# Kernel optimization log

Hardware: AMD Instinct MI355X
Metric: run time of the kernel (lower is better)

Reference implementation:

```python
import jax, jax.numpy as jnp
import numpy as np

B, T, N, D, NH = 4, 256, 8, 128, 4
SCALES = (1, 2, 3, 5)
LAGS = (1, 2, 3)
MLP_H = 32
NL_SCALE = 0.1
CMIN, CMAX = -2.5, 2.0
L_ENC = 2  # num_attn_layers


def _ln(x, g, b, eps=1e-5):
    m = x.mean(-1, keepdims=True)
    v = ((x - m) ** 2).mean(-1, keepdims=True)
    return (x - m) * jax.lax.rsqrt(v + eps) * g + b


def _gelu(x):
    return jax.nn.gelu(x, approximate=False)


def _mha(q, k, v, Wq, bq, Wk, bk, Wv, bv, Wo, bo, nh):
    Bq, Lq, Dm = q.shape
    Lk = k.shape[1]
    hd = Dm // nh
    qh = (q @ Wq.T + bq).reshape(Bq, Lq, nh, hd).transpose(0, 2, 1, 3)
    kh = (k @ Wk.T + bk).reshape(Bq, Lk, nh, hd).transpose(0, 2, 1, 3)
    vh = (v @ Wv.T + bv).reshape(Bq, Lk, nh, hd).transpose(0, 2, 1, 3)
    s = jnp.einsum('bhqd,bhkd->bhqk', qh, kh) / jnp.sqrt(jnp.float32(hd))
    p = jax.nn.softmax(s, axis=-1)
    o = jnp.einsum('bhqk,bhkd->bhqd', p, vh).transpose(0, 2, 1, 3).reshape(Bq, Lq, Dm)
    return o @ Wo.T + bo


def setup_inputs() -> dict:
    key = jax.random.key(0)
    ks = jax.random.split(key, 24)
    def w(k, shape, s=0.02):
        return s * jax.random.normal(k, shape, jnp.float32)
    inp = {}
    inp['visible_states'] = jax.random.uniform(ks[0], (B, T, N), jnp.float32) + 0.05
    inp['state_emb'] = jax.random.normal(ks[1], (B, T, N, D), jnp.float32)
    # LearnedBaseline params
    inp['r5'] = 0.1 * jnp.ones((N,), jnp.float32)
    A = 0.02 * jax.random.normal(ks[2], (N, N), jnp.float32)
    inp['A55'] = A.at[jnp.arange(N), jnp.arange(N)].set(-0.2)
    inp['bl_bias'] = jnp.zeros((N,), jnp.float32)
    inp['nl_W1'] = w(ks[3], (MLP_H, N), 0.1); inp['nl_b1'] = jnp.zeros((MLP_H,), jnp.float32)
    inp['nl_W2'] = w(ks[4], (N, MLP_H), 0.1); inp['nl_b2'] = jnp.zeros((N,), jnp.float32)
    # ResidualEncoder input MLP
    IN_DIM = len(SCALES) * (1 + len(LAGS))  # 16
    inp['mlp_W1'] = w(ks[5], (D, IN_DIM), 0.1); inp['mlp_b1'] = jnp.zeros((D,), jnp.float32)
    inp['mlp_W2'] = w(ks[6], (D, D)); inp['mlp_b2'] = jnp.zeros((D,), jnp.float32)
    inp['mlp_ln_g'] = jnp.ones((D,), jnp.float32); inp['mlp_ln_b'] = jnp.zeros((D,), jnp.float32)
    # ResidualEncoder transformer layers (stacked over L_ENC layers)
    inp['enc_qkv_W'] = w(ks[7], (L_ENC, 3 * D, D)); inp['enc_qkv_b'] = jnp.zeros((L_ENC, 3 * D), jnp.float32)
    inp['enc_out_W'] = w(ks[8], (L_ENC, D, D)); inp['enc_out_b'] = jnp.zeros((L_ENC, D), jnp.float32)
    inp['enc_ln1_g'] = jnp.ones((L_ENC, D), jnp.float32); inp['enc_ln1_b'] = jnp.zeros((L_ENC, D), jnp.float32)
    inp['enc_ff_W1'] = w(ks[9], (L_ENC, 2 * D, D)); inp['enc_ff_b1'] = jnp.zeros((L_ENC, 2 * D), jnp.float32)
    inp['enc_ff_W2'] = w(ks[10], (L_ENC, D, 2 * D)); inp['enc_ff_b2'] = jnp.zeros((L_ENC, D), jnp.float32)
    inp['enc_ln2_g'] = jnp.ones((L_ENC, D), jnp.float32); inp['enc_ln2_b'] = jnp.zeros((L_ENC, D), jnp.float32)
    # CrossAttentionFusion
    inp['ca_Wq'] = w(ks[11], (D, D)); inp['ca_bq'] = jnp.zeros((D,), jnp.float32)
    inp['ca_Wk'] = w(ks[12], (D, D)); inp['ca_bk'] = jnp.zeros((D,), jnp.float32)
    inp['ca_Wv'] = w(ks[13], (D, D)); inp['ca_bv'] = jnp.zeros((D,), jnp.float32)
    inp['ca_Wo'] = w(ks[14], (D, D)); inp['ca_bo'] = jnp.zeros((D,), jnp.float32)
    inp['ca_ln1_g'] = jnp.ones((D,), jnp.float32); inp['ca_ln1_b'] = jnp.zeros((D,), jnp.float32)
    inp['ca_ff_W1'] = w(ks[15], (4 * D, 2 * D)); inp['ca_ff_b1'] = jnp.zeros((4 * D,), jnp.float32)
    inp['ca_ff_W2'] = w(ks[16], (D, 4 * D)); inp['ca_ff_b2'] = jnp.zeros((D,), jnp.float32)
    inp['ca_ln2_g'] = jnp.ones((D,), jnp.float32); inp['ca_ln2_b'] = jnp.zeros((D,), jnp.float32)
    return inp


def _forward(visible_states, state_emb, r5, A55, bl_bias, nl_W1, nl_b1, nl_W2, nl_b2,
             mlp_W1, mlp_b1, mlp_W2, mlp_b2, mlp_ln_g, mlp_ln_b,
             enc_qkv_W, enc_qkv_b, enc_out_W, enc_out_b, enc_ln1_g, enc_ln1_b,
             enc_ff_W1, enc_ff_b1, enc_ff_W2, enc_ff_b2, enc_ln2_g, enc_ln2_b,
             ca_Wq, ca_bq, ca_Wk, ca_bk, ca_Wv, ca_bv, ca_Wo, ca_bo,
             ca_ln1_g, ca_ln1_b, ca_ff_W1, ca_ff_b1, ca_ff_W2, ca_ff_b2,
             ca_ln2_g, ca_ln2_b):
    # ---- LearnedBaseline on x_t = visible_states[:, :-1] ----
    safe = jnp.clip(visible_states, 1e-6, None)
    logx = jnp.log(safe)
    x_t = visible_states[:, :-1]  # (B,T-1,N)
    lin = r5 + jnp.einsum('btn,mn->btm', x_t, A55)
    nl = _gelu(x_t @ nl_W1.T + nl_b1) @ nl_W2.T + nl_b2
    b1 = lin + NL_SCALE * nl + bl_bias  # (B,T-1,N)
    # ---- MultiScaleResidual ----
    res_list = []
    for k in SCALES:
        actual = jnp.clip(logx[:, k:] - logx[:, :-k], CMIN * k, CMAX * k)  # (B,T-k,N)
        bk = b1[:, 0:T - k]
        for i in range(1, k):
            bk = bk + b1[:, i:i + T - k]
        res = actual - bk
        res_list.append(jnp.pad(res, ((0, 0), (0, k), (0, 0))))
    residuals = jnp.stack(res_list, axis=-1)  # (B,T,N,S)
    # ---- ResidualEncoder: takens delays ----
    feats = [residuals] + [jnp.pad(residuals, ((0, 0), (lag, 0), (0, 0), (0, 0)))[:, :T]
                           for lag in LAGS]
    x = jnp.concatenate(feats, axis=-1)  # (B,T,N,16)
    x = _gelu(x @ mlp_W1.T + mlp_b1)
    x = _gelu(x @ mlp_W2.T + mlp_b2)
    x = _ln(x, mlp_ln_g, mlp_ln_b)
    # sinusoidal PE over time
    pos = jnp.arange(T, dtype=jnp.float32)[:, None]
    div = jnp.exp(jnp.arange(0, D, 2, dtype=jnp.float32) * (-jnp.log(10000.0) / D))
    pe = jnp.stack([jnp.sin(pos * div), jnp.cos(pos * div)], axis=-1).reshape(T, D)
    x = x + pe[None, :, None, :]
    # temporal self-attention over (B*N, T, D)
    xt = x.transpose(0, 2, 1, 3).reshape(B * N, T, D)
    for i in range(L_ENC):
        Wq, Wk, Wv = jnp.split(enc_qkv_W[i], 3, axis=0)
        bq, bk_, bv = jnp.split(enc_qkv_b[i], 3)
        a = _mha(xt, xt, xt, Wq, bq, Wk, bk_, Wv, bv, enc_out_W[i], enc_out_b[i], NH)
        xt = _ln(xt + a, enc_ln1_g[i], enc_ln1_b[i])
        ff = _gelu(xt @ enc_ff_W1[i].T + enc_ff_b1[i]) @ enc_ff_W2[i].T + enc_ff_b2[i]
        xt = _ln(xt + ff, enc_ln2_g[i], enc_ln2_b[i])
    residual_emb = xt.reshape(B, N, T, D).transpose(0, 2, 1, 3)  # (B,T,N,D)
    # ---- CrossAttentionFusion ----
    s = state_emb.reshape(B, T * N, D)
    r = residual_emb.reshape(B, T * N, D)
    a = _mha(s, r, r, ca_Wq, ca_bq, ca_Wk, ca_bk, ca_Wv, ca_bv, ca_Wo, ca_bo, NH)
    s = _ln(s + a, ca_ln1_g, ca_ln1_b)
    fused = _gelu(jnp.concatenate([s, r], axis=-1) @ ca_ff_W1.T + ca_ff_b1) @ ca_ff_W2.T + ca_ff_b2
    out = _ln(s + fused, ca_ln2_g, ca_ln2_b)
    return out.reshape(B, T, N, D)


def reference(visible_states, state_emb, r5, A55, bl_bias, nl_W1, nl_b1, nl_W2, nl_b2,
              mlp_W1, mlp_b1, mlp_W2, mlp_b2, mlp_ln_g, mlp_ln_b,
              enc_qkv_W, enc_qkv_b, enc_out_W, enc_out_b, enc_ln1_g, enc_ln1_b,
              enc_ff_W1, enc_ff_b1, enc_ff_W2, enc_ff_b2, enc_ln2_g, enc_ln2_b,
              ca_Wq, ca_bq, ca_Wk, ca_bk, ca_Wv, ca_bv, ca_Wo, ca_bo,
              ca_ln1_g, ca_ln1_b, ca_ff_W1, ca_ff_b1, ca_ff_W2, ca_ff_b2,
              ca_ln2_g, ca_ln2_b):
    return _forward(visible_states, state_emb, r5, A55, bl_bias, nl_W1, nl_b1, nl_W2, nl_b2,
                    mlp_W1, mlp_b1, mlp_W2, mlp_b2, mlp_ln_g, mlp_ln_b,
                    enc_qkv_W, enc_qkv_b, enc_out_W, enc_out_b, enc_ln1_g, enc_ln1_b,
                    enc_ff_W1, enc_ff_b1, enc_ff_W2, enc_ff_b2, enc_ln2_g, enc_ln2_b,
                    ca_Wq, ca_bq, ca_Wk, ca_bk, ca_Wv, ca_bv, ca_Wo, ca_bo,
                    ca_ln1_g, ca_ln1_b, ca_ff_W1, ca_ff_b1, ca_ff_W2, ca_ff_b2,
                    ca_ln2_g, ca_ln2_b)
```

## Files before the change

kernel.cpp:

```cpp
#include <hip/hip_runtime.h>
#include <math.h>

#define B_ 4
#define T_ 256
#define N_ 8
#define D_ 128
#define NH_ 4
#define HD_ 32
#define LENC_ 2
#define MLPH_ 32
#define NL_SCALE_ 0.1f

typedef __bf16 bf16;
typedef __attribute__((ext_vector_type(2))) __bf16 bf16x2;
typedef __attribute__((ext_vector_type(4))) __bf16 bf16x4;
typedef __attribute__((ext_vector_type(8))) __bf16 bf16x8;
typedef __attribute__((ext_vector_type(4))) float f32x4;

__device__ __forceinline__ f32x4 pv_mfma16(bf16x4 a, bf16x4 b, f32x4 c) {
#if __has_builtin(__builtin_amdgcn_mfma_f32_16x16x16_bf16)
    return __builtin_amdgcn_mfma_f32_16x16x16_bf16(a, b, c, 0, 0, 0);
#else
    typedef __attribute__((ext_vector_type(4))) short s4;
    union U { bf16x4 h; s4 s; };
    U ua, ub; ua.h = a; ub.h = b;
    return __builtin_amdgcn_mfma_f32_16x16x16bf16_1k(ua.s, ub.s, c, 0, 0, 0);
#endif
}

__device__ __forceinline__ float gelu_f(float x) {
    return 0.5f * x * (1.0f + erff(x * 0.7071067811865476f));
}

__global__ void k_prep(const float* __restrict__ eqkvW, const float* __restrict__ eoutW,
                       const float* __restrict__ eff1, const float* __restrict__ eff2,
                       const float* __restrict__ wq, const float* __restrict__ wk,
                       const float* __restrict__ wv, const float* __restrict__ wo,
                       const float* __restrict__ cff1, const float* __restrict__ cff2,
                       const float* __restrict__ mlpW2, const float* __restrict__ semb,
                       const float* __restrict__ bk, const float* __restrict__ bv,
                       bf16* __restrict__ Wpk, bf16* __restrict__ sembh,
                       float* __restrict__ bpk) {
    int i = blockIdx.x * 256 + threadIdx.x;
    if (i < 540672) {
        const float* src; int off;
        if      (i < 98304)  { src = eqkvW; off = 0; }
        else if (i < 131072) { src = eoutW; off = 98304; }
        else if (i < 196608) { src = eff1;  off = 131072; }
        else if (i < 262144) { src = eff2;  off = 196608; }
        else if (i < 278528) { src = wq;    off = 262144; }
        else if (i < 294912) { src = wk;    off = 278528; }
        else if (i < 311296) { src = wv;    off = 294912; }
        else if (i < 327680) { src = wo;    off = 311296; }
        else if (i < 458752) { src = cff1;  off = 327680; }
        else if (i < 524288) { src = cff2;  off = 458752; }
        else                 { src = mlpW2; off = 524288; }
        Wpk[i] = (bf16)src[i - off];
    } else if (i < 540672 + 1048576) {
        int j = i - 540672;
        sembh[j] = (bf16)semb[j];
    } else if (i < 540672 + 1048576 + 256) {
        int t = i - 540672 - 1048576;
        bpk[t] = (t < 128) ? bk[t] : bv[t - 128];
    }
}

__global__ void k_b1(const float* __restrict__ vs, const float* __restrict__ r5,
                     const float* __restrict__ A55, const float* __restrict__ bl_bias,
                     const float* __restrict__ nlW1, const float* __restrict__ nlb1,
                     const float* __restrict__ nlW2, const float* __restrict__ nlb2,
                     float* __restrict__ b1w) {
    int idx = blockIdx.x * blockDim.x + threadIdx.x;
    if (idx >= B_ * (T_ - 1)) return;
    int b = idx / (T_ - 1), t = idx % (T_ - 1);
    float x[N_];
    for (int n = 0; n < N_; n++) x[n] = vs[(b * T_ + t) * N_ + n];
    float h[MLPH_];
    for (int j = 0; j < MLPH_; j++) {
        float a = nlb1[j];
        for (int n = 0; n < N_; n++) a += x[n] * nlW1[j * N_ + n];
        h[j] = gelu_f(a);
    }
    for (int m = 0; m < N_; m++) {
        float lin = r5[m];
        for (int n = 0; n < N_; n++) lin += x[n] * A55[m * N_ + n];
        float nl = nlb2[m];
        for (int j = 0; j < MLPH_; j++) nl += h[j] * nlW2[m * MLPH_ + j];
        b1w[idx * N_ + m] = lin + NL_SCALE_ * nl + bl_bias[m];
    }
}

__global__ void k_mlp1(const float* __restrict__ vs, const float* __restrict__ b1w,
                       const float* __restrict__ W1, const float* __restrict__ b1,
                       bf16* __restrict__ H1h) {
    int tok = blockIdx.x;
    int d = threadIdx.x;
    int b = tok >> 11, t = (tok >> 3) & 255, n = tok & 7;
    __shared__ float f[16];
    if (d < 16) {
        const int SC[4] = {1, 2, 3, 5};
        int lag = d >> 2, si = d & 3, k = SC[si];
        int tp = t - lag;
        float r = 0.0f;
        if (tp >= 0 && tp < T_ - k) {
            float lx0 = logf(fmaxf(vs[(b * T_ + tp) * N_ + n], 1e-6f));
            float lx1 = logf(fmaxf(vs[(b * T_ + tp + k) * N_ + n], 1e-6f));
            float a = lx1 - lx0;
            a = fminf(fmaxf(a, -2.5f * (float)k), 2.0f * (float)k);
            float bk = 0.0f;
            for (int i = 0; i < k; i++) bk += b1w[(b * (T_ - 1) + tp + i) * N_ + n];
            r = a - bk;
        }
        f[d] = r;
    }
    __syncthreads();
    float a = b1[d];
    const float* w = W1 + d * 16;
#pragma unroll
    for (int c = 0; c < 16; c++) a += f[c] * w[c];
    H1h[(size_t)tok * 128 + d] = (bf16)gelu_f(a);
}

__global__ __launch_bounds__(256) void k_gemm4(
    const bf16* __restrict__ A, const bf16* __restrict__ W,
    const float* __restrict__ bias, float* __restrict__ Cf,
    bf16* __restrict__ Ch, bf16* __restrict__ dq, bf16* __restrict__ dk,
    bf16* __restrict__ dvv, int M, int N, int K, int act, int mode) {
    int lane = threadIdx.x & 63;
    int wv = threadIdx.x >> 6;
    int c = lane & 15, g = lane >> 4;
    int nN = N >> 6;
    int tn = blockIdx.x % nN, tm = blockIdx.x / nN;
    int row0 = tm * 64 + wv * 16;
    int cb = tn * 64;

    const bf16x8* Ap  = (const bf16x8*)(A + (size_t)(row0 + c) * K) + g;
    const bf16x8* Wp0 = (const bf16x8*)(W + (size_t)(cb + c) * K) + g;
    const bf16x8* Wp1 = (const bf16x8*)(W + (size_t)(cb + 16 + c) * K) + g;
    const bf16x8* Wp2 = (const bf16x8*)(W + (size_t)(cb + 32 + c) * K) + g;
    const bf16x8* Wp3 = (const bf16x8*)(W + (size_t)(cb + 48 + c) * K) + g;
    f32x4 a0 = {0, 0, 0, 0}, a1 = {0, 0, 0, 0};
    f32x4 a2 = {0, 0, 0, 0}, a3 = {0, 0, 0, 0};
    int nk = K >> 5;
    for (int k = 0; k < nk; k++) {
        bf16x8 av = Ap[k * 4];
        a0 = __builtin_amdgcn_mfma_f32_16x16x32_bf16(av, Wp0[k * 4], a0, 0, 0, 0);
        a1 = __builtin_amdgcn_mfma_f32_16x16x32_bf16(av, Wp1[k * 4], a1, 0, 0, 0);
        a2 = __builtin_amdgcn_mfma_f32_16x16x32_bf16(av, Wp2[k * 4], a2, 0, 0, 0);
        a3 = __builtin_amdgcn_mfma_f32_16x16x32_bf16(av, Wp3[k * 4], a3, 0, 0, 0);
    }
    int rowb = row0 + g * 4;
#pragma unroll
    for (int ct = 0; ct < 4; ct++) {
        f32x4 acc = (ct == 0) ? a0 : (ct == 1) ? a1 : (ct == 2) ? a2 : a3;
        int col = cb + ct * 16 + c;
        float bvv = bias[col];
#pragma unroll
        for (int i = 0; i < 4; i++) {
            float v = acc[i] + bvv;
            if (act) v = gelu_f(v);
            int row = rowb + i;
            if (mode == 0) {
                if (Cf) Cf[(size_t)row * N + col] = v;
                if (Ch) Ch[(size_t)row * N + col] = (bf16)v;
            } else if (mode == 1) {
                int s = row >> 8, t = row & 255;
                int h = (col >> 5) & 3, d = col & 31;
                int sh = s * 4 + h;
                if (col < 128)      dq[((size_t)sh * 256 + t) * 32 + d] = (bf16)v;
                else if (col < 256) dk[((size_t)sh * 256 + t) * 32 + d] = (bf16)v;
                else                dvv[((size_t)sh * 32 + d) * 256 + t] = (bf16)v;
            } else if (mode == 2) {
                int b = row >> 11, ll = row & 2047;
                int h = col >> 5, d = col & 31;
                dq[((size_t)(b * 4 + h) * 2048 + ll) * 32 + d] = (bf16)v;
            } else {
                int b = row >> 11, n = (row >> 8) & 7, t = row & 255;
                int ll = t * 8 + n;
                int h = (col >> 5) & 3, d = col & 31;
                if (col < 128) dk[((size_t)(b * 4 + h) * 2048 + ll) * 32 + d] = (bf16)v;
                else           dvv[((size_t)(b * 4 + h) * 32 + d) * 2048 + ll] = (bf16)v;
            }
        }
    }
}

__global__ __launch_bounds__(256) void k_gemm_ln(
    const bf16* __restrict__ A, const bf16* __restrict__ W,
    const float* __restrict__ bias, int K,
    const float* __restrict__ resf,
    const float* __restrict__ g, const float* __restrict__ be,
    float* __restrict__ outf, bf16* __restrict__ outh, int hs,
    const bf16* __restrict__ catsrc, int flags) {
    __shared__ float S[32][132];
    int tid = threadIdx.x;
    int w = tid >> 6, lane = tid & 63;
    int c = lane & 15, gq = lane >> 4;
    int r0 = blockIdx.x * 32 + (w >> 1) * 16;
    int cb = (w & 1) * 64;

    const bf16x8* Ap  = (const bf16x8*)(A + (size_t)(r0 + c) * K) + gq;
    const bf16x8* Wp0 = (const bf16x8*)(W + (size_t)(cb + c) * K) + gq;
    const bf16x8* Wp1 = (const bf16x8*)(W + (size_t)(cb + 16 + c) * K) + gq;
    const bf16x8* Wp2 = (const bf16x8*)(W + (size_t)(cb + 32 + c) * K) + gq;
    const bf16x8* Wp3 = (const bf16x8*)(W + (size_t)(cb + 48 + c) * K) + gq;
    f32x4 a0 = {0, 0, 0, 0}, a1 = {0, 0, 0, 0};
    f32x4 a2 = {0, 0, 0, 0}, a3 = {0, 0, 0, 0};
    int nk = K >> 5;
    for (int k = 0; k < nk; k++) {
        bf16x8 av = Ap[k * 4];
        a0 = __builtin_amdgcn_mfma_f32_16x16x32_bf16(av, Wp0[k * 4], a0, 0, 0, 0);
        a1 = __builtin_amdgcn_mfma_f32_16x16x32_bf16(av, Wp1[k * 4], a1, 0, 0, 0);
        a2 = __builtin_amdgcn_mfma_f32_16x16x32_bf16(av, Wp2[k * 4], a2, 0, 0, 0);
        a3 = __builtin_amdgcn_mfma_f32_16x16x32_bf16(av, Wp3[k * 4], a3, 0, 0, 0);
    }
    int lrow = (w >> 1) * 16 + gq * 4;
    float b0 = bias[cb + c], b1v = bias[cb + 16 + c];
    float b2v = bias[cb + 32 + c], b3v = bias[cb + 48 + c];
#pragma unroll
    for (int r = 0; r < 4; r++) {
        float v0 = a0[r] + b0, v1 = a1[r] + b1v;
        float v2 = a2[r] + b2v, v3 = a3[r] + b3v;
        if (flags & 1) {
            v0 = gelu_f(v0); v1 = gelu_f(v1); v2 = gelu_f(v2); v3 = gelu_f(v3);
        }
        S[lrow + r][cb + c] = v0;       S[lrow + r][cb + 16 + c] = v1;
        S[lrow + r][cb + 32 + c] = v2;  S[lrow + r][cb + 48 + c] = v3;
    }
    __syncthreads();

    int row = tid >> 3, cg = tid & 7;
    int grow = blockIdx.x * 32 + row;
    int b = grow >> 11, t = (grow >> 3) & 255, n = grow & 7;
    int orow = (flags & 4) ? ((b * 8 + n) * 256 + t) : grow;
    float v[16];
#pragma unroll
    for (int j = 0; j < 16; j++) v[j] = S[row][cg * 16 + j];
    if (resf) {
        const float4* rp = (const float4*)(resf + (size_t)grow * 128 + cg * 16);
#pragma unroll
        for (int j4 = 0; j4 < 4; j4++) {
            float4 rv = rp[j4];
            v[4 * j4 + 0] += rv.x; v[4 * j4 + 1] += rv.y;
            v[4 * j4 + 2] += rv.z; v[4 * j4 + 3] += rv.w;
        }
    }
    float s = 0.0f;
#pragma unroll
    for (int j = 0; j < 16; j++) s += v[j];
    s += __shfl_xor(s, 1); s += __shfl_xor(s, 2); s += __shfl_xor(s, 4);
    float mean = s * (1.0f / 128.0f);
    float vs = 0.0f;
#pragma unroll
    for (int j = 0; j < 16; j++) { float d = v[j] - mean; vs += d * d; }
    vs += __shfl_xor(vs, 1); vs += __shfl_xor(vs, 2); vs += __shfl_xor(vs, 4);
    float rstd = rsqrtf(vs * (1.0f / 128.0f) + 1e-5f);
    float y[16];
#pragma unroll
    for (int j = 0; j < 16; j++) {
        int col = cg * 16 + j;
        y[j] = (v[j] - mean) * rstd * g[col] + be[col];
    }
    if (flags & 2) {
#pragma unroll
        for (int jj = 0; jj < 8; jj++) {
            int j2 = cg * 8 + jj;
            float freq = expf((float)(2 * j2) * (-9.210340371976184f / 128.0f));
            float ang = (float)t * freq;
            y[2 * jj] += sinf(ang);
            y[2 * jj + 1] += cosf(ang);
        }
    }
    if (outf) {
        float4* op = (float4*)(outf + (size_t)orow * 128 + cg * 16);
#pragma unroll
        for (int j4 = 0; j4 < 4; j4++) {
            float4 o; o.x = y[4 * j4]; o.y = y[4 * j4 + 1];
            o.z = y[4 * j4 + 2]; o.w = y[4 * j4 + 3];
            op[j4] = o;
        }
    }
    if (outh) {
        bf16x8* op = (bf16x8*)(outh + (size_t)orow * hs + cg * 16);
#pragma unroll
        for (int j8 = 0; j8 < 2; j8++) {
            bf16x8 o;
#pragma unroll
            for (int e = 0; e < 8; e++) o[e] = (bf16)y[8 * j8 + e];
            op[j8] = o;
        }
        if (catsrc) {
            const bf16x8* cp = (const bf16x8*)(
                catsrc + ((size_t)(b * 8 + n) * 256 + t) * 128 + cg * 16);
            bf16x8* dp = (bf16x8*)(outh + (size_t)orow * 256 + 128 + cg * 16);
            dp[0] = cp[0]; dp[1] = cp[1];
        }
    }
}

__global__ __launch_bounds__(256) void k_mattn(
    const bf16* __restrict__ Qh, const bf16* __restrict__ Kh,
    const bf16* __restrict__ Vth, bf16* __restrict__ ATTh,
    int Lq, int Lk, int NSH) {
    int sh = blockIdx.x % NSH;
    int qblk = blockIdx.x / NSH;
    int wv = threadIdx.x >> 6;
    int lane = threadIdx.x & 63;
    int c = lane & 15, g = lane >> 4;
    int q0 = qblk * 64;

    __shared__ float O_lds[4][64][36];
    __shared__ float L_lds[4][64];

    const float scale = 0.17677669529663687f;
    const f32x4 zero = {0, 0, 0, 0};

    bf16x8 bq[4];
#pragma unroll
    for (int qt = 0; qt < 4; qt++)
        bq[qt] = *(const bf16x8*)(
            Qh + ((size_t)sh * Lq + q0 + qt * 16 + c) * 32 + g * 8);

    int klen = Lk >> 2;
    int kbeg = wv * klen;
    const bf16* Kbase = Kh + (size_t)sh * Lk * 32 + (size_t)kbeg * 32;
    const bf16* Vbase = Vth + (size_t)sh * 32 * Lk + kbeg;

    f32x4 oT[4][2];
#pragma unroll
    for (int qt = 0; qt < 4; qt++) { oT[qt][0] = zero; oT[qt][1] = zero; }
    float lsum[4] = {0, 0, 0, 0};

    int ntiles = klen >> 5;
    bf16x8 ka = *(const bf16x8*)(Kbase + (size_t)c * 32 + g * 8);
    bf16x8 kb = *(const bf16x8*)(Kbase + (size_t)(16 + c) * 32 + g * 8);
    bf16x4 va0 = *(const bf16x4*)(Vbase + (size_t)c * Lk + g * 4);
    bf16x4 va1 = *(const bf16x4*)(Vbase + (size_t)c * Lk + 16 + g * 4);
    bf16x4 vb0 = *(const bf16x4*)(Vbase + (size_t)(16 + c) * Lk + g * 4);
    bf16x4 vb1 = *(const bf16x4*)(Vbase + (size_t)(16 + c) * Lk + 16 + g * 4);

    for (int t = 0; t < ntiles; t++) {
        bf16x8 cka = ka, ckb = kb;
        bf16x4 cva0 = va0, cva1 = va1, cvb0 = vb0, cvb1 = vb1;
        int nk0 = ((t + 1 < ntiles) ? (t + 1) : t) << 5;
        ka = *(const bf16x8*)(Kbase + (size_t)(nk0 + c) * 32 + g * 8);
        kb = *(const bf16x8*)(Kbase + (size_t)(nk0 + 16 + c) * 32 + g * 8);
        va0 = *(const bf16x4*)(Vbase + (size_t)c * Lk + nk0 + g * 4);
        va1 = *(const bf16x4*)(Vbase + (size_t)c * Lk + nk0 + 16 + g * 4);
        vb0 = *(const bf16x4*)(Vbase + (size_t)(16 + c) * Lk + nk0 + g * 4);
        vb1 = *(const bf16x4*)(Vbase + (size_t)(16 + c) * Lk + nk0 + 16 + g * 4);

#pragma unroll
        for (int qt = 0; qt < 4; qt++) {
            f32x4 s0 = __builtin_amdgcn_mfma_f32_16x16x32_bf16(cka, bq[qt], zero, 0, 0, 0);
            f32x4 s1 = __builtin_amdgcn_mfma_f32_16x16x32_bf16(ckb, bq[qt], zero, 0, 0, 0);
            bf16x4 p0, p1;
#pragma unroll
            for (int r = 0; r < 4; r++) {
                float e0 = __expf(s0[r] * scale);
                float e1 = __expf(s1[r] * scale);
                lsum[qt] += e0 + e1;
                p0[r] = (bf16)e0;
                p1[r] = (bf16)e1;
            }
            oT[qt][0] = pv_mfma16(cva0, p0, oT[qt][0]);
            oT[qt][0] = pv_mfma16(cva1, p1, oT[qt][0]);
            oT[qt][1] = pv_mfma16(cvb0, p0, oT[qt][1]);
            oT[qt][1] = pv_mfma16(cvb1, p1, oT[qt][1]);
        }
    }

#pragma unroll
    for (int qt = 0; qt < 4; qt++) {
        float s = lsum[qt];
        s += __shfl_xor(s, 16);
        s += __shfl_xor(s, 32);
        if (g == 0) L_lds[wv][qt * 16 + c] = s;
        *(f32x4*)&O_lds[wv][qt * 16 + c][g * 4] = oT[qt][0];
        *(f32x4*)&O_lds[wv][qt * 16 + c][16 + g * 4] = oT[qt][1];
    }
    __syncthreads();

    int tid = threadIdx.x;
    int ql = tid >> 2, dq = (tid & 3) * 8;
    float ltot = L_lds[0][ql] + L_lds[1][ql] + L_lds[2][ql] + L_lds[3][ql];
    float inv = 1.0f / ltot;
    float acc[8];
#pragma unroll
    for (int j = 0; j < 8; j++) acc[j] = 0.0f;
#pragma unroll
    for (int w = 0; w < 4; w++) {
        const float* p = &O_lds[w][ql][dq];
#pragma unroll
        for (int j = 0; j < 8; j++) acc[j] += p[j];
    }
    int h = sh & 3, sb = sh >> 2;
    bf16x8 o;
#pragma unroll
    for (int j = 0; j < 8; j++) o[j] = (bf16)(acc[j] * inv);
    *(bf16x8*)(ATTh + ((size_t)sb * Lq + q0 + ql) * 128 + h * 32 + dq) = o;
}

extern "C" void kernel_launch(void* const* d_in, const int* in_sizes, int n_in,
                              void* d_out, int out_size, void* d_ws, size_t ws_size,
                              hipStream_t stream) {
    const float* vs       = (const float*)d_in[0];
    const float* semb     = (const float*)d_in[1];
    const float* r5       = (const float*)d_in[2];
    const float* A55      = (const float*)d_in[3];
    const float* bl_bias  = (const float*)d_in[4];
    const float* nl_W1    = (const float*)d_in[5];
    const float* nl_b1    = (const float*)d_in[6];
    const float* nl_W2    = (const float*)d_in[7];
    const float* nl_b2    = (const float*)d_in[8];
    const float* mlp_W1   = (const float*)d_in[9];
    const float* mlp_b1   = (const float*)d_in[10];
    const float* mlp_W2   = (const float*)d_in[11];
    const float* mlp_b2   = (const float*)d_in[12];
    const float* mlp_ln_g = (const float*)d_in[13];
    const float* mlp_ln_b = (const float*)d_in[14];
    const float* enc_qkv_W = (const float*)d_in[15];
    const float* enc_qkv_b = (const float*)d_in[16];
    const float* enc_out_W = (const float*)d_in[17];
    const float* enc_out_b = (const float*)d_in[18];
    const float* enc_ln1_g = (const float*)d_in[19];
    const float* enc_ln1_b = (const float*)d_in[20];
    const float* enc_ff_W1 = (const float*)d_in[21];
    const float* enc_ff_b1 = (const float*)d_in[22];
    const float* enc_ff_W2 = (const float*)d_in[23];
    const float* enc_ff_b2 = (const float*)d_in[24];
    const float* enc_ln2_g = (const float*)d_in[25];
    const float* enc_ln2_b = (const float*)d_in[26];
    const float* ca_Wq = (const float*)d_in[27];
    const float* ca_bq = (const float*)d_in[28];
    const float* ca_Wk = (const float*)d_in[29];
    const float* ca_bk = (const float*)d_in[30];
    const float* ca_Wv = (const float*)d_in[31];
    const float* ca_bv = (const float*)d_in[32];
    const float* ca_Wo = (const float*)d_in[33];
    const float* ca_bo = (const float*)d_in[34];
    const float* ca_ln1_g = (const float*)d_in[35];
    const float* ca_ln1_b = (const float*)d_in[36];
    const float* ca_ff_W1 = (const float*)d_in[37];
    const float* ca_ff_b1 = (const float*)d_in[38];
    const float* ca_ff_W2 = (const float*)d_in[39];
    const float* ca_ff_b2 = (const float*)d_in[40];
    const float* ca_ln2_g = (const float*)d_in[41];
    const float* ca_ln2_b = (const float*)d_in[42];
    float* out = (float*)d_out;

    char* base = (char*)d_ws;
    float* b1w   = (float*)(base + 0);
    float* X0    = (float*)(base + 163840);
    float* X1    = (float*)(base + 4358144);
    char*  QKVr  = base + 8552448;
    bf16*  Wpk   = (bf16*) (base + 25329664);
    float* bpk   = (float*)(base + 26411008);
    bf16*  X0h   = (bf16*) (base + 26412032);
    bf16*  X1h   = (bf16*) (base + 28509184);
    bf16*  sembh = (bf16*) (base + 30606336);
    bf16*  ATTh  = (bf16*) (base + 32703488);
    bf16*  Qh    = (bf16*)QKVr;
    bf16*  Kh    = (bf16*)(QKVr + 2097152);
    bf16*  Vth   = (bf16*)(QKVr + 4194304);
    bf16*  CATh  = (bf16*)QKVr;
    bf16*  Hh    = (bf16*)(QKVr + 4194304);

    const int NTOK = B_ * T_ * N_;

    k_prep<<<dim3(6209), dim3(256), 0, stream>>>(
        enc_qkv_W, enc_out_W, enc_ff_W1, enc_ff_W2, ca_Wq, ca_Wk, ca_Wv, ca_Wo,
        ca_ff_W1, ca_ff_W2, mlp_W2, semb, ca_bk, ca_bv, Wpk, sembh, bpk);

    k_b1<<<dim3((B_ * (T_ - 1) + 63) / 64), dim3(64), 0, stream>>>(
        vs, r5, A55, bl_bias, nl_W1, nl_b1, nl_W2, nl_b2, b1w);
    k_mlp1<<<dim3(NTOK), dim3(128), 0, stream>>>(vs, b1w, mlp_W1, mlp_b1,
                                                 (bf16*)X1h);
    k_gemm_ln<<<dim3(256), dim3(256), 0, stream>>>(
        (bf16*)X1h, Wpk + 524288, mlp_b2, 128, nullptr, mlp_ln_g, mlp_ln_b,
        X0, X0h, 128, nullptr, 1 | 2 | 4);

    for (int i = 0; i < LENC_; i++) {
        k_gemm4<<<dim3(768), dim3(256), 0, stream>>>(
            X0h, Wpk + i * 49152, enc_qkv_b + i * 384, nullptr, nullptr,
            Qh, Kh, Vth, NTOK, 384, 128, 0, 1);
        k_mattn<<<dim3(512), dim3(256), 0, stream>>>(
            Qh, Kh, Vth, ATTh, 256, 256, 128);
        k_gemm_ln<<<dim3(256), dim3(256), 0, stream>>>(
            ATTh, Wpk + 98304 + i * 16384, enc_out_b + i * 128, 128, X0,
            enc_ln1_g + i * 128, enc_ln1_b + i * 128, X1, X1h, 128, nullptr, 0);
        k_gemm4<<<dim3(512), dim3(256), 0, stream>>>(
            X1h, Wpk + 131072 + i * 32768, enc_ff_b1 + i * 256, nullptr, Hh,
            nullptr, nullptr, nullptr, NTOK, 256, 128, 1, 0);
        k_gemm_ln<<<dim3(256), dim3(256), 0, stream>>>(
            Hh, Wpk + 196608 + i * 32768, enc_ff_b2 + i * 128, 256, X1,
            enc_ln2_g + i * 128, enc_ln2_b + i * 128, X0, X0h, 128, nullptr, 0);
    }

    k_gemm4<<<dim3(256), dim3(256), 0, stream>>>(
        sembh, Wpk + 262144, ca_bq, nullptr, nullptr, Qh, nullptr, nullptr,
        NTOK, 128, 128, 0, 2);
    k_gemm4<<<dim3(512), dim3(256), 0, stream>>>(
        X0h, Wpk + 278528, bpk, nullptr, nullptr, nullptr, Kh, Vth,
        NTOK, 256, 128, 0, 3);
    k_mattn<<<dim3(512), dim3(256), 0, stream>>>(
        Qh, Kh, Vth, ATTh, 2048, 2048, 16);
    k_gemm_ln<<<dim3(256), dim3(256), 0, stream>>>(
        ATTh, Wpk + 311296, ca_bo, 128, semb, ca_ln1_g, ca_ln1_b,
        X1, CATh, 256, X0h, 0);
    k_gemm4<<<dim3(1024), dim3(256), 0, stream>>>(
        CATh, Wpk + 327680, ca_ff_b1, nullptr, Hh, nullptr, nullptr, nullptr,
        NTOK, 512, 256, 1, 0);
    k_gemm_ln<<<dim3(256), dim3(256), 0, stream>>>(
        Hh, Wpk + 458752, ca_ff_b2, 512, X1, ca_ln2_g, ca_ln2_b,
        out, nullptr, 128, nullptr, 0);
}
```

Before: 373.9 us.

## Fuse attention output, LayerNorm and FFN into single per-tile tail kernels

Each encoder layer's out-projection, residual LayerNorm, FFN up-projection with GELU, down-projection and second LayerNorm now run in one kernel per 32-row tile, with intermediates held in shared memory rather than written to global buffers. The cross-attention tail gets the same treatment, building the concatenated FFN input in registers from the LN output and the encoder output. The cross-attention Q and KV projections are merged into one launch as well. This removes several kernel launches and global round trips of the hidden activations. In exchange, each tile's FFN weights are reread by every block, shared-memory use per block is higher, and only 256 blocks do the larger FFN GEMMs, so parallelism drops. The cross tail's second residual now uses the bf16 copy of the LN output rather than the fp32 one.

```diff
diff --git a/kernel.cpp b/kernel.cpp
--- a/kernel.cpp
+++ b/kernel.cpp
@@ -121,16 +121,16 @@
     H1h[(size_t)tok * 128 + d] = (bf16)gelu_f(a);
 }
 
-__global__ __launch_bounds__(256) void k_gemm4(
-    const bf16* __restrict__ A, const bf16* __restrict__ W,
+__device__ __forceinline__ void gemm4_body(
+    int bid, const bf16* __restrict__ A, const bf16* __restrict__ W,
     const float* __restrict__ bias, float* __restrict__ Cf,
     bf16* __restrict__ Ch, bf16* __restrict__ dq, bf16* __restrict__ dk,
-    bf16* __restrict__ dvv, int M, int N, int K, int act, int mode) {
+    bf16* __restrict__ dvv, int N, int K, int act, int mode) {
     int lane = threadIdx.x & 63;
     int wv = threadIdx.x >> 6;
     int c = lane & 15, g = lane >> 4;
     int nN = N >> 6;
-    int tn = blockIdx.x % nN, tm = blockIdx.x / nN;
+    int tn = bid % nN, tm = bid / nN;
     int row0 = tm * 64 + wv * 16;
     int cb = tn * 64;
 
@@ -185,13 +185,33 @@
     }
 }
 
+__global__ __launch_bounds__(256) void k_gemm4(
+    const bf16* __restrict__ A, const bf16* __restrict__ W,
+    const float* __restrict__ bias, bf16* __restrict__ dq,
+    bf16* __restrict__ dk, bf16* __restrict__ dvv, int N, int K, int mode) {
+    gemm4_body(blockIdx.x, A, W, bias, nullptr, nullptr, dq, dk, dvv,
+               N, K, 0, mode);
+}
+
+__global__ __launch_bounds__(256) void k_qkvc(
+    const bf16* __restrict__ sembh, const bf16* __restrict__ Wq,
+    const float* __restrict__ bq, const bf16* __restrict__ X0h,
+    const bf16* __restrict__ Wkv, const float* __restrict__ bkv,
+    bf16* __restrict__ Qh, bf16* __restrict__ Kh, bf16* __restrict__ Vth) {
+    if (blockIdx.x < 256)
+        gemm4_body(blockIdx.x, sembh, Wq, bq, nullptr, nullptr,
+                   Qh, nullptr, nullptr, 128, 128, 0, 2);
+    else
+        gemm4_body(blockIdx.x - 256, X0h, Wkv, bkv, nullptr, nullptr,
+                   nullptr, Kh, Vth, 256, 128, 0, 3);
+}
+
 __global__ __launch_bounds__(256) void k_gemm_ln(
     const bf16* __restrict__ A, const bf16* __restrict__ W,
     const float* __restrict__ bias, int K,
     const float* __restrict__ resf,
     const float* __restrict__ g, const float* __restrict__ be,
-    float* __restrict__ outf, bf16* __restrict__ outh, int hs,
-    const bf16* __restrict__ catsrc, int flags) {
+    float* __restrict__ outf, bf16* __restrict__ outh, int hs, int flags) {
     __shared__ float S[32][132];
     int tid = threadIdx.x;
     int w = tid >> 6, lane = tid & 63;
@@ -289,11 +309,357 @@
             for (int e = 0; e < 8; e++) o[e] = (bf16)y[8 * j8 + e];
             op[j8] = o;
         }
-        if (catsrc) {
-            const bf16x8* cp = (const bf16x8*)(
-                catsrc + ((size_t)(b * 8 + n) * 256 + t) * 128 + cg * 16);
-            bf16x8* dp = (bf16x8*)(outh + (size_t)orow * 256 + 128 + cg * 16);
-            dp[0] = cp[0]; dp[1] = cp[1];
+    }
+}
+
+__global__ __launch_bounds__(256) void k_enc_tail(
+    const bf16* __restrict__ ATTh, const bf16* __restrict__ Wo,
+    const float* __restrict__ bo, const float* __restrict__ X0res,
+    const float* __restrict__ g1, const float* __restrict__ be1,
+    const bf16* __restrict__ W1, const float* __restrict__ bf1,
+    const bf16* __restrict__ W2, const float* __restrict__ bf2,
+    const float* __restrict__ g2, const float* __restrict__ be2,
+    float* __restrict__ X0out, bf16* __restrict__ X0hout) {
+    __shared__ float S[32][132];
+    __shared__ float X1f[32][132];
+    __shared__ bf16 X1h[32][136];
+    __shared__ bf16 H[32][264];
+    int tid = threadIdx.x;
+    int w = tid >> 6, lane = tid & 63;
+    int c = lane & 15, gq = lane >> 4;
+    int r0l = (w >> 1) * 16;
+    int cb = (w & 1) * 64;
+    int blk = blockIdx.x;
+    const f32x4 zero = {0, 0, 0, 0};
+
+    {
+        const bf16x8* Ap  = (const bf16x8*)(ATTh + (size_t)(blk * 32 + r0l + c) * 128) + gq;
+        const bf16x8* Wp0 = (const bf16x8*)(Wo + (size_t)(cb + c) * 128) + gq;
+        const bf16x8* Wp1 = (const bf16x8*)(Wo + (size_t)(cb + 16 + c) * 128) + gq;
+        const bf16x8* Wp2 = (const bf16x8*)(Wo + (size_t)(cb + 32 + c) * 128) + gq;
+        const bf16x8* Wp3 = (const bf16x8*)(Wo + (size_t)(cb + 48 + c) * 128) + gq;
+        f32x4 a0 = zero, a1 = zero, a2 = zero, a3 = zero;
+#pragma unroll
+        for (int k = 0; k < 4; k++) {
+            bf16x8 av = Ap[k * 4];
+            a0 = __builtin_amdgcn_mfma_f32_16x16x32_bf16(av, Wp0[k * 4], a0, 0, 0, 0);
+            a1 = __builtin_amdgcn_mfma_f32_16x16x32_bf16(av, Wp1[k * 4], a1, 0, 0, 0);
+            a2 = __builtin_amdgcn_mfma_f32_16x16x32_bf16(av, Wp2[k * 4], a2, 0, 0, 0);
+            a3 = __builtin_amdgcn_mfma_f32_16x16x32_bf16(av, Wp3[k * 4], a3, 0, 0, 0);
+        }
+        int lrow = r0l + gq * 4;
+        float b0 = bo[cb + c], b1v = bo[cb + 16 + c];
+        float b2v = bo[cb + 32 + c], b3v = bo[cb + 48 + c];
+#pragma unroll
+        for (int r = 0; r < 4; r++) {
+            S[lrow + r][cb + c] = a0[r] + b0;
+            S[lrow + r][cb + 16 + c] = a1[r] + b1v;
+            S[lrow + r][cb + 32 + c] = a2[r] + b2v;
+            S[lrow + r][cb + 48 + c] = a3[r] + b3v;
+        }
+    }
+    __syncthreads();
+    {
+        int row = tid >> 3, cg = tid & 7;
+        float v[16];
+        const float4* rp = (const float4*)(X0res + (size_t)(blk * 32 + row) * 128 + cg * 16);
+#pragma unroll
+        for (int j4 = 0; j4 < 4; j4++) {
+            float4 rv = rp[j4];
+            v[4 * j4 + 0] = S[row][cg * 16 + 4 * j4 + 0] + rv.x;
+            v[4 * j4 + 1] = S[row][cg * 16 + 4 * j4 + 1] + rv.y;
+            v[4 * j4 + 2] = S[row][cg * 16 + 4 * j4 + 2] + rv.z;
+            v[4 * j4 + 3] = S[row][cg * 16 + 4 * j4 + 3] + rv.w;
+        }
+        float s = 0.0f;
+#pragma unroll
+        for (int j = 0; j < 16; j++) s += v[j];
+        s += __shfl_xor(s, 1); s += __shfl_xor(s, 2); s += __shfl_xor(s, 4);
+        float mean = s * (1.0f / 128.0f);
+        float vs = 0.0f;
+#pragma unroll
+        for (int j = 0; j < 16; j++) { float d = v[j] - mean; vs += d * d; }
+        vs += __shfl_xor(vs, 1); vs += __shfl_xor(vs, 2); vs += __shfl_xor(vs, 4);
+        float rstd = rsqrtf(vs * (1.0f / 128.0f) + 1e-5f);
+#pragma unroll
+        for (int j = 0; j < 16; j++) {
+            int col = cg * 16 + j;
+            float y = (v[j] - mean) * rstd * g1[col] + be1[col];
+            X1f[row][col] = y;
+            X1h[row][col] = (bf16)y;
+        }
+    }
+    __syncthreads();
+    {
+        bf16x8 af[4];
+#pragma unroll
+        for (int k = 0; k < 4; k++)
+            af[k] = *(const bf16x8*)&X1h[r0l + c][k * 32 + gq * 8];
+#pragma unroll
+        for (int ci = 0; ci < 2; ci++) {
+            int cb2 = cb + ci * 128;
+            const bf16x8* Wp0 = (const bf16x8*)(W1 + (size_t)(cb2 + c) * 128) + gq;
+            const bf16x8* Wp1 = (const bf16x8*)(W1 + (size_t)(cb2 + 16 + c) * 128) + gq;
+            const bf16x8* Wp2 = (const bf16x8*)(W1 + (size_t)(cb2 + 32 + c) * 128) + gq;
+            const bf16x8* Wp3 = (const bf16x8*)(W1 + (size_t)(cb2 + 48 + c) * 128) + gq;
+            f32x4 a0 = zero, a1 = zero, a2 = zero, a3 = zero;
+#pragma unroll
+            for (int k = 0; k < 4; k++) {
+                a0 = __builtin_amdgcn_mfma_f32_16x16x32_bf16(af[k], Wp0[k * 4], a0, 0, 0, 0);
+                a1 = __builtin_amdgcn_mfma_f32_16x16x32_bf16(af[k], Wp1[k * 4], a1, 0, 0, 0);
+                a2 = __builtin_amdgcn_mfma_f32_16x16x32_bf16(af[k], Wp2[k * 4], a2, 0, 0, 0);
+                a3 = __builtin_amdgcn_mfma_f32_16x16x32_bf16(af[k], Wp3[k * 4], a3, 0, 0, 0);
+            }
+            int lrow = r0l + gq * 4;
+#pragma unroll
+            for (int r = 0; r < 4; r++) {
+                H[lrow + r][cb2 + c]      = (bf16)gelu_f(a0[r] + bf1[cb2 + c]);
+                H[lrow + r][cb2 + 16 + c] = (bf16)gelu_f(a1[r] + bf1[cb2 + 16 + c]);
+                H[lrow + r][cb2 + 32 + c] = (bf16)gelu_f(a2[r] + bf1[cb2 + 32 + c]);
+                H[lrow + r][cb2 + 48 + c] = (bf16)gelu_f(a3[r] + bf1[cb2 + 48 + c]);
+            }
+        }
+    }
+    __syncthreads();
+    {
+        bf16x8 af[8];
+#pragma unroll
+        for (int k = 0; k < 8; k++)
+            af[k] = *(const bf16x8*)&H[r0l + c][k * 32 + gq * 8];
+        const bf16x8* Wp0 = (const bf16x8*)(W2 + (size_t)(cb + c) * 256) + gq;
+        const bf16x8* Wp1 = (const bf16x8*)(W2 + (size_t)(cb + 16 + c) * 256) + gq;
+        const bf16x8* Wp2 = (const bf16x8*)(W2 + (size_t)(cb + 32 + c) * 256) + gq;
+        const bf16x8* Wp3 = (const bf16x8*)(W2 + (size_t)(cb + 48 + c) * 256) + gq;
+        f32x4 a0 = zero, a1 = zero, a2 = zero, a3 = zero;
+#pragma unroll
+        for (int k = 0; k < 8; k++) {
+            a0 = __builtin_amdgcn_mfma_f32_16x16x32_bf16(af[k], Wp0[k * 4], a0, 0, 0, 0);
+            a1 = __builtin_amdgcn_mfma_f32_16x16x32_bf16(af[k], Wp1[k * 4], a1, 0, 0, 0);
+            a2 = __builtin_amdgcn_mfma_f32_16x16x32_bf16(af[k], Wp2[k * 4], a2, 0, 0, 0);
+            a3 = __builtin_amdgcn_mfma_f32_16x16x32_bf16(af[k], Wp3[k * 4], a3, 0, 0, 0);
+        }
+        int lrow = r0l + gq * 4;
+        float b0 = bf2[cb + c], b1v = bf2[cb + 16 + c];
+        float b2v = bf2[cb + 32 + c], b3v = bf2[cb + 48 + c];
+#pragma unroll
+        for (int r = 0; r < 4; r++) {
+            S[lrow + r][cb + c] = a0[r] + b0;
+            S[lrow + r][cb + 16 + c] = a1[r] + b1v;
+            S[lrow + r][cb + 32 + c] = a2[r] + b2v;
+            S[lrow + r][cb + 48 + c] = a3[r] + b3v;
+        }
+    }
+    __syncthreads();
+    {
+        int row = tid >> 3, cg = tid & 7;
+        float v[16];
+#pragma unroll
+        for (int j = 0; j < 16; j++)
+            v[j] = S[row][cg * 16 + j] + X1f[row][cg * 16 + j];
+        float s = 0.0f;
+#pragma unroll
+        for (int j = 0; j < 16; j++) s += v[j];
+        s += __shfl_xor(s, 1); s += __shfl_xor(s, 2); s += __shfl_xor(s, 4);
+        float mean = s * (1.0f / 128.0f);
+        float vs = 0.0f;
+#pragma unroll
+        for (int j = 0; j < 16; j++) { float d = v[j] - mean; vs += d * d; }
+        vs += __shfl_xor(vs, 1); vs += __shfl_xor(vs, 2); vs += __shfl_xor(vs, 4);
+        float rstd = rsqrtf(vs * (1.0f / 128.0f) + 1e-5f);
+        size_t grow = (size_t)(blk * 32 + row);
+        float4* of = (float4*)(X0out + grow * 128 + cg * 16);
+        bf16x8* oh = (bf16x8*)(X0hout + grow * 128 + cg * 16);
+        float y[16];
+#pragma unroll
+        for (int j = 0; j < 16; j++) {
+            int col = cg * 16 + j;
+            y[j] = (v[j] - mean) * rstd * g2[col] + be2[col];
+        }
+#pragma unroll
+        for (int j4 = 0; j4 < 4; j4++) {
+            float4 o; o.x = y[4 * j4]; o.y = y[4 * j4 + 1];
+            o.z = y[4 * j4 + 2]; o.w = y[4 * j4 + 3];
+            of[j4] = o;
+        }
+#pragma unroll
+        for (int j8 = 0; j8 < 2; j8++) {
+            bf16x8 o;
+#pragma unroll
+            for (int e = 0; e < 8; e++) o[e] = (bf16)y[8 * j8 + e];
+            oh[j8] = o;
+        }
+    }
+}
+
+__global__ __launch_bounds__(256) void k_cross_tail(
+    const bf16* __restrict__ ATTh, const bf16* __restrict__ Wo,
+    const float* __restrict__ bo, const float* __restrict__ semb,
+    const float* __restrict__ g1, const float* __restrict__ be1,
+    const bf16* __restrict__ X0h, const bf16* __restrict__ W1,
+    const float* __restrict__ bf1, const bf16* __restrict__ W2,
+    const float* __restrict__ bf2, const float* __restrict__ g2,
+    const float* __restrict__ be2, float* __restrict__ outp) {
+    __shared__ float S[32][132];
+    __shared__ bf16 s1h[32][136];
+    __shared__ bf16 H[32][520];
+    int tid = threadIdx.x;
+    int w = tid >> 6, lane = tid & 63;
+    int c = lane & 15, gq = lane >> 4;
+    int r0l = (w >> 1) * 16;
+    int cb = (w & 1) * 64;
+    int blk = blockIdx.x;
+    const f32x4 zero = {0, 0, 0, 0};
+
+    bf16x8 agl[4];
+    {
+        int tr = blk * 32 + r0l + c;
+        int b = tr >> 11, t = (tr >> 3) & 255, n = tr & 7;
+        const bf16* xrow = X0h + ((size_t)((b * 8 + n) * 256 + t)) * 128;
+#pragma unroll
+        for (int k = 0; k < 4; k++)
+            agl[k] = *(const bf16x8*)(xrow + k * 32 + gq * 8);
+    }
+
+    {
+        const bf16x8* Ap  = (const bf16x8*)(ATTh + (size_t)(blk * 32 + r0l + c) * 128) + gq;
+        const bf16x8* Wp0 = (const bf16x8*)(Wo + (size_t)(cb + c) * 128) + gq;
+        const bf16x8* Wp1 = (const bf16x8*)(Wo + (size_t)(cb + 16 + c) * 128) + gq;
+        const bf16x8* Wp2 = (const bf16x8*)(Wo + (size_t)(cb + 32 + c) * 128) + gq;
+        const bf16x8* Wp3 = (const bf16x8*)(Wo + (size_t)(cb + 48 + c) * 128) + gq;
+        f32x4 a0 = zero, a1 = zero, a2 = zero, a3 = zero;
+#pragma unroll
+        for (int k = 0; k < 4; k++) {
+            bf16x8 av = Ap[k * 4];
+            a0 = __builtin_amdgcn_mfma_f32_16x16x32_bf16(av, Wp0[k * 4], a0, 0, 0, 0);
+            a1 = __builtin_amdgcn_mfma_f32_16x16x32_bf16(av, Wp1[k * 4], a1, 0, 0, 0);
+            a2 = __builtin_amdgcn_mfma_f32_16x16x32_bf16(av, Wp2[k * 4], a2, 0, 0, 0);
+            a3 = __builtin_amdgcn_mfma_f32_16x16x32_bf16(av, Wp3[k * 4], a3, 0, 0, 0);
+        }
+        int lrow = r0l + gq * 4;
+        float b0 = bo[cb + c], b1v = bo[cb + 16 + c];
+        float b2v = bo[cb + 32 + c], b3v = bo[cb + 48 + c];
+#pragma unroll
+        for (int r = 0; r < 4; r++) {
+            S[lrow + r][cb + c] = a0[r] + b0;
+            S[lrow + r][cb + 16 + c] = a1[r] + b1v;
+            S[lrow + r][cb + 32 + c] = a2[r] + b2v;
+            S[lrow + r][cb + 48 + c] = a3[r] + b3v;
+        }
+    }
+    __syncthreads();
+    {
+        int row = tid >> 3, cg = tid & 7;
+        float v[16];
+        const float4* rp = (const float4*)(semb + (size_t)(blk * 32 + row) * 128 + cg * 16);
+#pragma unroll
+        for (int j4 = 0; j4 < 4; j4++) {
+            float4 rv = rp[j4];
+            v[4 * j4 + 0] = S[row][cg * 16 + 4 * j4 + 0] + rv.x;
+            v[4 * j4 + 1] = S[row][cg * 16 + 4 * j4 + 1] + rv.y;
+            v[4 * j4 + 2] = S[row][cg * 16 + 4 * j4 + 2] + rv.z;
+            v[4 * j4 + 3] = S[row][cg * 16 + 4 * j4 + 3] + rv.w;
+        }
+        float s = 0.0f;
+#pragma unroll
+        for (int j = 0; j < 16; j++) s += v[j];
+        s += __shfl_xor(s, 1); s += __shfl_xor(s, 2); s += __shfl_xor(s, 4);
+        float mean = s * (1.0f / 128.0f);
+        float vs = 0.0f;
+#pragma unroll
+        for (int j = 0; j < 16; j++) { float d = v[j] - mean; vs += d * d; }
+        vs += __shfl_xor(vs, 1); vs += __shfl_xor(vs, 2); vs += __shfl_xor(vs, 4);
+        float rstd = rsqrtf(vs * (1.0f / 128.0f) + 1e-5f);
+#pragma unroll
+        for (int j = 0; j < 16; j++) {
+            int col = cg * 16 + j;
+            s1h[row][col] = (bf16)((v[j] - mean) * rstd * g1[col] + be1[col]);
+        }
+    }
+    __syncthreads();
+    {
+        bf16x8 afl[4];
+#pragma unroll
+        for (int k = 0; k < 4; k++)
+            afl[k] = *(const bf16x8*)&s1h[r0l + c][k * 32 + gq * 8];
+#pragma unroll
+        for (int ci = 0; ci < 4; ci++) {
+            int cb2 = cb + ci * 128;
+            const bf16x8* Wp0 = (const bf16x8*)(W1 + (size_t)(cb2 + c) * 256) + gq;
+            const bf16x8* Wp1 = (const bf16x8*)(W1 + (size_t)(cb2 + 16 + c) * 256) + gq;
+            const bf16x8* Wp2 = (const bf16x8*)(W1 + (size_t)(cb2 + 32 + c) * 256) + gq;
+            const bf16x8* Wp3 = (const bf16x8*)(W1 + (size_t)(cb2 + 48 + c) * 256) + gq;
+            f32x4 a0 = zero, a1 = zero, a2 = zero, a3 = zero;
+#pragma unroll
+            for (int k = 0; k < 8; k++) {
+                bf16x8 av = (k < 4) ? afl[k] : agl[k - 4];
+                a0 = __builtin_amdgcn_mfma_f32_16x16x32_bf16(av, Wp0[k * 4], a0, 0, 0, 0);
+                a1 = __builtin_amdgcn_mfma_f32_16x16x32_bf16(av, Wp1[k * 4], a1, 0, 0, 0);
+                a2 = __builtin_amdgcn_mfma_f32_16x16x32_bf16(av, Wp2[k * 4], a2, 0, 0, 0);
+                a3 = __builtin_amdgcn_mfma_f32_16x16x32_bf16(av, Wp3[k * 4], a3, 0, 0, 0);
+            }
+            int lrow = r0l + gq * 4;
+#pragma unroll
+            for (int r = 0; r < 4; r++) {
+                H[lrow + r][cb2 + c]      = (bf16)gelu_f(a0[r] + bf1[cb2 + c]);
+                H[lrow + r][cb2 + 16 + c] = (bf16)gelu_f(a1[r] + bf1[cb2 + 16 + c]);
+                H[lrow + r][cb2 + 32 + c] = (bf16)gelu_f(a2[r] + bf1[cb2 + 32 + c]);
+                H[lrow + r][cb2 + 48 + c] = (bf16)gelu_f(a3[r] + bf1[cb2 + 48 + c]);
+            }
+        }
+    }
+    __syncthreads();
+    {
+        const bf16x8* Wp0 = (const bf16x8*)(W2 + (size_t)(cb + c) * 512) + gq;
+        const bf16x8* Wp1 = (const bf16x8*)(W2 + (size_t)(cb + 16 + c) * 512) + gq;
+        const bf16x8* Wp2 = (const bf16x8*)(W2 + (size_t)(cb + 32 + c) * 512) + gq;
+        const bf16x8* Wp3 = (const bf16x8*)(W2 + (size_t)(cb + 48 + c) * 512) + gq;
+        f32x4 a0 = zero, a1 = zero, a2 = zero, a3 = zero;
+#pragma unroll
+        for (int k = 0; k < 16; k++) {
+            bf16x8 av = *(const bf16x8*)&H[r0l + c][k * 32 + gq * 8];
+            a0 = __builtin_amdgcn_mfma_f32_16x16x32_bf16(av, Wp0[k * 4], a0, 0, 0, 0);
+            a1 = __builtin_amdgcn_mfma_f32_16x16x32_bf16(av, Wp1[k * 4], a1, 0, 0, 0);
+            a2 = __builtin_amdgcn_mfma_f32_16x16x32_bf16(av, Wp2[k * 4], a2, 0, 0, 0);
+            a3 = __builtin_amdgcn_mfma_f32_16x16x32_bf16(av, Wp3[k * 4], a3, 0, 0, 0);
+        }
+        int lrow = r0l + gq * 4;
+        float b0 = bf2[cb + c], b1v = bf2[cb + 16 + c];
+        float b2v = bf2[cb + 32 + c], b3v = bf2[cb + 48 + c];
+#pragma unroll
+        for (int r = 0; r < 4; r++) {
+            S[lrow + r][cb + c] = a0[r] + b0;
+            S[lrow + r][cb + 16 + c] = a1[r] + b1v;
+            S[lrow + r][cb + 32 + c] = a2[r] + b2v;
+            S[lrow + r][cb + 48 + c] = a3[r] + b3v;
+        }
+    }
+    __syncthreads();
+    {
+        int row = tid >> 3, cg = tid & 7;
+        float v[16];
+#pragma unroll
+        for (int j = 0; j < 16; j++)
+            v[j] = S[row][cg * 16 + j] + (float)s1h[row][cg * 16 + j];
+        float s = 0.0f;
+#pragma unroll
+        for (int j = 0; j < 16; j++) s += v[j];
+        s += __shfl_xor(s, 1); s += __shfl_xor(s, 2); s += __shfl_xor(s, 4);
+        float mean = s * (1.0f / 128.0f);
+        float vs = 0.0f;
+#pragma unroll
+        for (int j = 0; j < 16; j++) { float d = v[j] - mean; vs += d * d; }
+        vs += __shfl_xor(vs, 1); vs += __shfl_xor(vs, 2); vs += __shfl_xor(vs, 4);
+        float rstd = rsqrtf(vs * (1.0f / 128.0f) + 1e-5f);
+        float4* of = (float4*)(outp + (size_t)(blk * 32 + row) * 128 + cg * 16);
+#pragma unroll
+        for (int j4 = 0; j4 < 4; j4++) {
+            float4 o;
+#pragma unroll
+            for (int e = 0; e < 4; e++) {
+                int col = cg * 16 + 4 * j4 + e;
+                ((float*)&o)[e] = (v[4 * j4 + e] - mean) * rstd * g2[col] + be2[col];
+            }
+            of[j4] = o;
         }
     }
 }
@@ -452,7 +818,6 @@
     char* base = (char*)d_ws;
     float* b1w   = (float*)(base + 0);
     float* X0    = (float*)(base + 163840);
-    float* X1    = (float*)(base + 4358144);
     char*  QKVr  = base + 8552448;
     bf16*  Wpk   = (bf16*) (base + 25329664);
     float* bpk   = (float*)(base + 26411008);
@@ -463,8 +828,6 @@
     bf16*  Qh    = (bf16*)QKVr;
     bf16*  Kh    = (bf16*)(QKVr + 2097152);
     bf16*  Vth   = (bf16*)(QKVr + 4194304);
-    bf16*  CATh  = (bf16*)QKVr;
-    bf16*  Hh    = (bf16*)(QKVr + 4194304);
 
     const int NTOK = B_ * T_ * N_;
 
@@ -474,44 +837,30 @@
 
     k_b1<<<dim3((B_ * (T_ - 1) + 63) / 64), dim3(64), 0, stream>>>(
         vs, r5, A55, bl_bias, nl_W1, nl_b1, nl_W2, nl_b2, b1w);
-    k_mlp1<<<dim3(NTOK), dim3(128), 0, stream>>>(vs, b1w, mlp_W1, mlp_b1,
-                                                 (bf16*)X1h);
+    k_mlp1<<<dim3(NTOK), dim3(128), 0, stream>>>(vs, b1w, mlp_W1, mlp_b1, X1h);
     k_gemm_ln<<<dim3(256), dim3(256), 0, stream>>>(
-        (bf16*)X1h, Wpk + 524288, mlp_b2, 128, nullptr, mlp_ln_g, mlp_ln_b,
-        X0, X0h, 128, nullptr, 1 | 2 | 4);
+        X1h, Wpk + 524288, mlp_b2, 128, nullptr, mlp_ln_g, mlp_ln_b,
+        X0, X0h, 128, 1 | 2 | 4);
 
     for (int i = 0; i < LENC_; i++) {
         k_gemm4<<<dim3(768), dim3(256), 0, stream>>>(
-            X0h, Wpk + i * 49152, enc_qkv_b + i * 384, nullptr, nullptr,
-            Qh, Kh, Vth, NTOK, 384, 128, 0, 1);
+            X0h, Wpk + i * 49152, enc_qkv_b + i * 384, Qh, Kh, Vth, 384, 128, 1);
         k_mattn<<<dim3(512), dim3(256), 0, stream>>>(
             Qh, Kh, Vth, ATTh, 256, 256, 128);
-        k_gemm_ln<<<dim3(256), dim3(256), 0, stream>>>(
-            ATTh, Wpk + 98304 + i * 16384, enc_out_b + i * 128, 128, X0,
-            enc_ln1_g + i * 128, enc_ln1_b + i * 128, X1, X1h, 128, nullptr, 0);
-        k_gemm4<<<dim3(512), dim3(256), 0, stream>>>(
-            X1h, Wpk + 131072 + i * 32768, enc_ff_b1 + i * 256, nullptr, Hh,
-            nullptr, nullptr, nullptr, NTOK, 256, 128, 1, 0);
-        k_gemm_ln<<<dim3(256), dim3(256), 0, stream>>>(
-            Hh, Wpk + 196608 + i * 32768, enc_ff_b2 + i * 128, 256, X1,
-            enc_ln2_g + i * 128, enc_ln2_b + i * 128, X0, X0h, 128, nullptr, 0);
-    }
-
-    k_gemm4<<<dim3(256), dim3(256), 0, stream>>>(
-        sembh, Wpk + 262144, ca_bq, nullptr, nullptr, Qh, nullptr, nullptr,
-        NTOK, 128, 128, 0, 2);
-    k_gemm4<<<dim3(512), dim3(256), 0, stream>>>(
-        X0h, Wpk + 278528, bpk, nullptr, nullptr, nullptr, Kh, Vth,
-        NTOK, 256, 128, 0, 3);
+        k_enc_tail<<<dim3(256), dim3(256), 0, stream>>>(
+            ATTh, Wpk + 98304 + i * 16384, enc_out_b + i * 128, X0,
+            enc_ln1_g + i * 128, enc_ln1_b + i * 128,
+            Wpk + 131072 + i * 32768, enc_ff_b1 + i * 256,
+            Wpk + 196608 + i * 32768, enc_ff_b2 + i * 128,
+            enc_ln2_g + i * 128, enc_ln2_b + i * 128, X0, X0h);
+    }
+
+    k_qkvc<<<dim3(768), dim3(256), 0, stream>>>(
+        sembh, Wpk + 262144, ca_bq, X0h, Wpk + 278528, bpk, Qh, Kh, Vth);
     k_mattn<<<dim3(512), dim3(256), 0, stream>>>(
         Qh, Kh, Vth, ATTh, 2048, 2048, 16);
-    k_gemm_ln<<<dim3(256), dim3(256), 0, stream>>>(
-        ATTh, Wpk + 311296, ca_bo, 128, semb, ca_ln1_g, ca_ln1_b,
-        X1, CATh, 256, X0h, 0);
-    k_gemm4<<<dim3(1024), dim3(256), 0, stream>>>(
-        CATh, Wpk + 327680, ca_ff_b1, nullptr, Hh, nullptr, nullptr, nullptr,
-        NTOK, 512, 256, 1, 0);
-    k_gemm_ln<<<dim3(256), dim3(256), 0, stream>>>(
-        Hh, Wpk + 458752, ca_ff_b2, 512, X1, ca_ln2_g, ca_ln2_b,
-        out, nullptr, 128, nullptr, 0);
-}
+    k_cross_tail<<<dim3(256), dim3(256), 0, stream>>>(
+        ATTh, Wpk + 311296, ca_bo, semb, ca_ln1_g, ca_ln1_b, X0h,
+        Wpk + 327680, ca_ff_b1, Wpk + 458752, ca_ff_b2,
+        ca_ln2_g, ca_ln2_b, out);
+}
```

Result: faster. 338.2 us (-9.5%).
